# Optimization experiments

Measured on AMD Instinct MI355X. Metric: run time of the kernel, lower is better.

The kernel has to match this reference:

```python
import jax, jax.numpy as jnp
import numpy as np

K = 16  # kNN neighbors


def _knn(xb, k):
    # xb: [N, H] -> [N, k] nearest-neighbor indices (self excluded)
    sq = jnp.sum(xb * xb, axis=-1)
    d = sq[:, None] + sq[None, :] - 2.0 * (xb @ xb.T)  # squared distances [N, N]
    n = xb.shape[0]
    big = jnp.asarray(1e30, d.dtype)
    d = d + jnp.eye(n, dtype=d.dtype) * big  # mask self-loops
    _, idx = jax.lax.top_k(-d, k)
    return idx


def _edgeconv(h, W0, b0, W1, b1, k):
    # Dynamic kNN graph on current features + EdgeConv with 2-layer MLP, aggr='add'
    idx = jax.vmap(lambda xb: _knn(xb, k))(h)                 # [B, N, k]
    xj = jax.vmap(lambda xb, ib: xb[ib])(h, idx)              # [B, N, k, H] gather neighbors
    xi = jnp.broadcast_to(h[:, :, None, :], xj.shape)         # [B, N, k, H]
    m = jnp.concatenate([xi, xj - xi], axis=-1)               # [B, N, k, 2H]
    e = jax.nn.elu(m @ W0 + b0)
    e = jax.nn.elu(e @ W1 + b1)
    return jnp.sum(e, axis=2)                                 # 'add' aggregation over neighbors


def _forward(x, W_in0, b_in0, W_in1, b_in1, W_in2, b_in2,
             W_e0, b_e0, W_e1, b_e1,
             W_o0, b_o0, W_o1, b_o1, W_o2, b_o2):
    # input network (in_layers=3)
    h = jax.nn.elu(x @ W_in0 + b_in0)
    h = jax.nn.elu(h @ W_in1 + b_in1)
    h = jax.nn.elu(h @ W_in2 + b_in2)
    # agg_layers=2 blocks of dynamic-kNN EdgeConv
    for l in range(W_e0.shape[0]):
        h = _edgeconv(h, W_e0[l], b_e0[l], W_e1[l], b_e1[l], K)
    # global max pool over nodes of each graph (pool='max')
    g = jnp.max(h, axis=1)                                    # [B, H]
    # output network (out_layers=3)
    g = jax.nn.elu(g @ W_o0 + b_o0)
    g = jax.nn.elu(g @ W_o1 + b_o1)
    logits = g @ W_o2 + b_o2
    return jax.nn.log_softmax(logits, axis=1)


def setup_inputs() -> dict:
    key = jax.random.key(0)
    ks = jax.random.split(key, 8)
    B, N, F, H, C, A = 128, 512, 5, 64, 10, 2
    s = jnp.float32(0.1)

    def w(k, shape):
        return jax.random.normal(k, shape, jnp.float32) * s

    return {
        'x': jax.random.normal(ks[0], (B, N, F), jnp.float32),
        'W_in0': w(ks[1], (F, H)), 'b_in0': jnp.zeros((H,), jnp.float32),
        'W_in1': w(ks[2], (H, H)), 'b_in1': jnp.zeros((H,), jnp.float32),
        'W_in2': w(ks[3], (H, H)), 'b_in2': jnp.zeros((H,), jnp.float32),
        'W_e0': w(ks[4], (A, 2 * H, H)), 'b_e0': jnp.zeros((A, H), jnp.float32),
        'W_e1': w(ks[5], (A, H, H)), 'b_e1': jnp.zeros((A, H), jnp.float32),
        'W_o0': w(ks[6], (H, H)), 'b_o0': jnp.zeros((H,), jnp.float32),
        'W_o1': w(ks[7], (H, H)), 'b_o1': jnp.zeros((H,), jnp.float32),
        'W_o2': w(jax.random.fold_in(key, 99), (H, C)), 'b_o2': jnp.zeros((C,), jnp.float32),
    }


def reference(x, W_in0, b_in0, W_in1, b_in1, W_in2, b_in2,
              W_e0, b_e0, W_e1, b_e1,
              W_o0, b_o0, W_o1, b_o1, W_o2, b_o2):
    return _forward(x, W_in0, b_in0, W_in1, b_in1, W_in2, b_in2,
                    W_e0, b_e0, W_e1, b_e1,
                    W_o0, b_o0, W_o1, b_o1, W_o2, b_o2)
```

## Files before the change

kernel.cpp:

```cpp
#include <hip/hip_runtime.h>
#include <hip/hip_fp16.h>
#include <cmath>

typedef _Float16 f16;
typedef _Float16 f16x8 __attribute__((ext_vector_type(8)));
typedef float f32x4 __attribute__((ext_vector_type(4)));

#define B_ 128
#define N_ 512
#define H_ 64
#define K_ 16

__device__ __forceinline__ float elu_(float x) { return x > 0.f ? x : (__expf(x) - 1.f); }
__device__ __forceinline__ unsigned umin_(unsigned a, unsigned b) { return a < b ? a : b; }
__device__ __forceinline__ unsigned umax_(unsigned a, unsigned b) { return a > b ? a : b; }
__device__ __forceinline__ f32x4 mfma16(f16x8 a, f16x8 b, f32x4 c) {
    return __builtin_amdgcn_mfma_f32_16x16x32_f16(a, b, c, 0, 0, 0);
}
__device__ __forceinline__ f32x4 splat4(float v) { f32x4 r; r[0]=v; r[1]=v; r[2]=v; r[3]=v; return r; }
__device__ __forceinline__ unsigned mbcnt_(unsigned long long mask) {
    return __builtin_amdgcn_mbcnt_hi((unsigned)(mask >> 32),
           __builtin_amdgcn_mbcnt_lo((unsigned)mask, 0u));
}
__device__ __forceinline__ f16 hexp_(f16 x) {
    __half h = *(__half*)&x; h = hexp(h); return *(f16*)&h;
}
__device__ __forceinline__ f16x8 elu8h_(f16x8 x) {
    f16x8 z; f16x8 one;
    #pragma unroll
    for (int i = 0; i < 8; ++i) { z[i] = (f16)0.f; one[i] = (f16)1.f; }
    f16x8 mx = __builtin_elementwise_max(x, z);
    f16x8 mn = __builtin_elementwise_min(x, z);
    f16x8 e;
    #pragma unroll
    for (int i = 0; i < 8; ++i) e[i] = hexp_(mn[i]);
    return mx + e - one;
}
__device__ __forceinline__ unsigned wmax64_(unsigned v) {
    v = umax_(v, (unsigned)__builtin_amdgcn_update_dpp(0, (int)v, 0x111, 0xf, 0xf, true));
    v = umax_(v, (unsigned)__builtin_amdgcn_update_dpp(0, (int)v, 0x112, 0xf, 0xf, true));
    v = umax_(v, (unsigned)__builtin_amdgcn_update_dpp(0, (int)v, 0x114, 0xf, 0xf, true));
    v = umax_(v, (unsigned)__builtin_amdgcn_update_dpp(0, (int)v, 0x118, 0xf, 0xf, true));
    v = umax_(v, (unsigned)__builtin_amdgcn_update_dpp(0, (int)v, 0x142, 0xa, 0xf, true));
    v = umax_(v, (unsigned)__builtin_amdgcn_update_dpp(0, (int)v, 0x143, 0xc, 0xf, true));
    return (unsigned)__builtin_amdgcn_readlane((int)v, 63);
}
__device__ __forceinline__ float rsum16lo_(float x) {
    x += __int_as_float(__builtin_amdgcn_update_dpp(0, __float_as_int(x), 0x101, 0xf, 0xf, true));
    x += __int_as_float(__builtin_amdgcn_update_dpp(0, __float_as_int(x), 0x102, 0xf, 0xf, true));
    x += __int_as_float(__builtin_amdgcn_update_dpp(0, __float_as_int(x), 0x104, 0xf, 0xf, true));
    x += __int_as_float(__builtin_amdgcn_update_dpp(0, __float_as_int(x), 0x108, 0xf, 0xf, true));
    return x;
}

__global__ __launch_bounds__(256) void mlp_kernel(const float* __restrict__ x,
        const float* __restrict__ W0, const float* __restrict__ b0,
        const float* __restrict__ W1, const float* __restrict__ b1,
        const float* __restrict__ W2, const float* __restrict__ b2,
        f16* __restrict__ hout, float* __restrict__ sqout)
{
    __shared__ f16 tile[4][16*72];
    const int lane = threadIdx.x & 63, wid = threadIdx.x >> 6;
    const int m = lane & 15, q = lane >> 4;
    const int rowbase = blockIdx.x*64 + wid*16;
    f16* tw = tile[wid];

    f16x8 af0, af1;
    {
        const float* xp = x + (size_t)(rowbase + m)*5;
        #pragma unroll
        for (int jj = 0; jj < 8; ++jj) { int k = q*8+jj; af0[jj] = (k < 5) ? (f16)xp[k] : (f16)0.f; }
    }
    f32x4 acc[4];
    #pragma unroll
    for (int t = 0; t < 4; ++t) {
        f16x8 bf;
        #pragma unroll
        for (int jj = 0; jj < 8; ++jj) { int k = q*8+jj; bf[jj] = (k < 5) ? (f16)W0[k*64 + t*16+m] : (f16)0.f; }
        acc[t] = splat4(b0[t*16+m]);
        acc[t] = mfma16(af0, bf, acc[t]);
    }
    #pragma unroll
    for (int t = 0; t < 4; ++t)
        #pragma unroll
        for (int r = 0; r < 4; ++r)
            tw[(q*4+r)*72 + t*16+m] = (f16)elu_(acc[t][r]);
    __syncthreads();
    af0 = *(const f16x8*)(tw + m*72 + q*8);
    af1 = *(const f16x8*)(tw + m*72 + q*8 + 32);
    __syncthreads();

    #pragma unroll
    for (int t = 0; t < 4; ++t) {
        f16x8 bfa, bfb;
        #pragma unroll
        for (int jj = 0; jj < 8; ++jj) {
            bfa[jj] = (f16)W1[(q*8+jj)*64 + t*16+m];
            bfb[jj] = (f16)W1[(q*8+jj+32)*64 + t*16+m];
        }
        acc[t] = splat4(b1[t*16+m]);
        acc[t] = mfma16(af0, bfa, acc[t]);
        acc[t] = mfma16(af1, bfb, acc[t]);
    }
    #pragma unroll
    for (int t = 0; t < 4; ++t)
        #pragma unroll
        for (int r = 0; r < 4; ++r)
            tw[(q*4+r)*72 + t*16+m] = (f16)elu_(acc[t][r]);
    __syncthreads();
    af0 = *(const f16x8*)(tw + m*72 + q*8);
    af1 = *(const f16x8*)(tw + m*72 + q*8 + 32);

    #pragma unroll
    for (int t = 0; t < 4; ++t) {
        f16x8 bfa, bfb;
        #pragma unroll
        for (int jj = 0; jj < 8; ++jj) {
            bfa[jj] = (f16)W2[(q*8+jj)*64 + t*16+m];
            bfb[jj] = (f16)W2[(q*8+jj+32)*64 + t*16+m];
        }
        acc[t] = splat4(b2[t*16+m]);
        acc[t] = mfma16(af0, bfa, acc[t]);
        acc[t] = mfma16(af1, bfb, acc[t]);
    }
    float s[4] = {0.f,0.f,0.f,0.f};
    #pragma unroll
    for (int t = 0; t < 4; ++t)
        #pragma unroll
        for (int r = 0; r < 4; ++r) {
            float v = elu_(acc[t][r]);
            hout[(size_t)(rowbase + q*4 + r)*64 + t*16 + m] = (f16)v;
            s[r] += v*v;
        }
    #pragma unroll
    for (int r = 0; r < 4; ++r) s[r] = rsum16lo_(s[r]);
    if (m == 0) {
        #pragma unroll
        for (int r = 0; r < 4; ++r) sqout[rowbase + q*4 + r] = s[r];
    }
}

__global__ __launch_bounds__(512, 8) void knn_kernel(const f16* __restrict__ hin,
        const float* __restrict__ sq, int* __restrict__ idxout,
        const float* __restrict__ We, const float* __restrict__ be,
        f16* __restrict__ Pout, f16* __restrict__ Qout)
{
    __shared__ unsigned keys[16*512];
    const int lane = threadIdx.x & 63;
    const int wid  = threadIdx.x >> 6;
    const int m = lane & 15, q = lane >> 4;
    const int b  = blockIdx.x >> 5;
    const int rt = blockIdx.x & 31;
    const int rowbase = rt*16;
    const f16* hb = hin + (size_t)b*N_*H_;
    const float* sqb = sq + b*N_;

    f16x8 af0, af1;
    {
        const f16* Ap = hb + (size_t)(rowbase + m)*64 + q*8;
        af0 = *(const f16x8*)Ap;
        af1 = *(const f16x8*)(Ap + 32);
    }
    const int colb0 = wid*16;
    f16x8 bf0[4], bf1[4];
    float sc[4];
    #pragma unroll
    for (int cti = 0; cti < 4; ++cti) {
        const f16* Bp = hb + (size_t)(colb0 + cti*128 + m)*64 + q*8;
        bf0[cti] = *(const f16x8*)Bp;
        bf1[cti] = *(const f16x8*)(Bp + 32);
        sc[cti] = sqb[colb0 + cti*128 + m];
    }
    int base_r[4];
    #pragma unroll
    for (int r = 0; r < 4; ++r) {
        const int row = q*4 + r;
        base_r[r] = row*512 + ((colb0 + m) ^ (row << 1));
    }
    #pragma unroll
    for (int cti = 0; cti < 4; ++cti) {
        f32x4 acc = splat4(0.f);
        acc = mfma16(af0, bf0[cti], acc);
        acc = mfma16(af1, bf1[cti], acc);
        #pragma unroll
        for (int r = 0; r < 4; ++r) {
            float d = fmaf(-2.f, acc[r], sc[cti]);
            unsigned u = __float_as_uint(d);
            u ^= (0x80000000u | (unsigned)((int)u >> 31));
            unsigned key = (u & 0xFFFFFE00u) | (unsigned)(colb0 + cti*128 + m);
            keys[base_r[r] + cti*128] = key;
        }
    }
    __syncthreads();

    unsigned kk[2][8];
    #pragma unroll
    for (int rr = 0; rr < 2; ++rr) {
        const int ri = wid*2 + rr;
        *(uint4*)&kk[rr][0] = *(const uint4*)(keys + ri*512 + lane*4);
        *(uint4*)&kk[rr][4] = *(const uint4*)(keys + ri*512 + 256 + lane*4);
    }
    unsigned* scr = keys + wid*2*512;

    unsigned v[2];
    #pragma unroll
    for (int rr = 0; rr < 2; ++rr) {
        unsigned mn = kk[rr][0];
        #pragma unroll
        for (int s2 = 1; s2 < 8; ++s2) mn = umin_(mn, kk[rr][s2]);
        v[rr] = mn;
    }
    unsigned T[2] = {0u,0u};
    #pragma unroll
    for (int bit = 31; bit >= 9; --bit) {
        #pragma unroll
        for (int rr = 0; rr < 2; ++rr) {
            unsigned cand = T[rr] | (1u << bit);
            int c = __popcll(__ballot(v[rr] < cand));
            T[rr] = (c < 17) ? cand : T[rr];
        }
    }
    T[0] |= 511u; T[1] |= 511u;

    unsigned cnt[2];
    #pragma unroll
    for (int rr = 0; rr < 2; ++rr) {
        unsigned long long bal[8];
        #pragma unroll
        for (int s2 = 0; s2 < 8; ++s2) bal[s2] = __ballot(kk[rr][s2] <= T[rr]);
        unsigned base = 0;
        #pragma unroll
        for (int s2 = 0; s2 < 8; ++s2) {
            if (kk[rr][s2] <= T[rr]) {
                unsigned pos = base + mbcnt_(bal[s2]);
                if (pos < 64u) scr[rr*64 + pos] = kk[rr][s2];
            }
            base += (unsigned)__popcll(bal[s2]);
        }
        cnt[rr] = base;
    }

    #pragma unroll
    for (int rr = 0; rr < 2; ++rr) {
        const unsigned cc_ = umin_(cnt[rr], 64u);
        const int ri = wid*2 + rr;
        const unsigned rowglob = (unsigned)(rowbase + ri);
        bool act = lane < (int)cc_;
        unsigned mv = act ? scr[rr*64 + lane] : 0u;
        if (act && (mv & 511u) == rowglob) { act = false; mv = 0u; }
        int e = __popcll(__ballot(act)) - 16;
        while (e > 0) {
            unsigned mx = wmax64_(mv);
            if (mv == mx) { act = false; mv = 0u; }
            --e;
        }
        int* outp = idxout + ((size_t)b*N_ + rowglob)*K_;
        unsigned long long bal = __ballot(act);
        unsigned rank = mbcnt_(bal);
        if (act) outp[rank] = (int)(mv & 511u);
    }

    {
        const int t = wid & 3;
        f32x4 acc = (wid < 4) ? splat4(be[t*16+m]) : splat4(0.f);
        #pragma unroll
        for (int cc = 0; cc < 2; ++cc) {
            const f16x8 afc = cc ? af1 : af0;
            f16x8 bb;
            if (wid < 4) {
                #pragma unroll
                for (int jj = 0; jj < 8; ++jj) {
                    float wa = We[(q*8+jj+32*cc)*64 + t*16+m];
                    float wb = We[(q*8+jj+32*cc+64)*64 + t*16+m];
                    bb[jj] = (f16)(wa - wb);
                }
            } else {
                #pragma unroll
                for (int jj = 0; jj < 8; ++jj)
                    bb[jj] = (f16)We[(q*8+jj+32*cc+64)*64 + t*16+m];
            }
            acc = mfma16(afc, bb, acc);
        }
        f16* outp = (wid < 4) ? Pout : Qout;
        #pragma unroll
        for (int r = 0; r < 4; ++r)
            outp[((size_t)b*N_ + rowbase + q*4 + r)*64 + t*16 + m] = (f16)acc[r];
    }
}

__device__ __forceinline__ void edge_node_(size_t r0, f16x8 pa, f16x8 pb,
        f16x8 qa, f16x8 qb, const f16x8 (&bf)[2][4], const float (&bcol)[4],
        f16* __restrict__ out, float* __restrict__ sqout, int lane)
{
    f16x8 af0 = elu8h_(pa + qa);
    f16x8 af1 = elu8h_(pb + qb);
    f32x4 acc[4];
    #pragma unroll
    for (int t = 0; t < 4; ++t) acc[t] = splat4(bcol[t]);
    #pragma unroll
    for (int t = 0; t < 4; ++t) acc[t] = mfma16(af0, bf[0][t], acc[t]);
    #pragma unroll
    for (int t = 0; t < 4; ++t) acc[t] = mfma16(af1, bf[1][t], acc[t]);
    float ssum = 0.f;
    #pragma unroll
    for (int t = 0; t < 4; ++t) {
        float s = elu_(acc[t][0]) + elu_(acc[t][1]) + elu_(acc[t][2]) + elu_(acc[t][3]);
        s += __shfl_xor(s, 16);
        s += __shfl_xor(s, 32);
        if (lane < 16) out[r0*64 + t*16 + lane] = (f16)s;
        ssum += s*s;
    }
    ssum = rsum16lo_(ssum);
    if (lane == 0) sqout[r0] = ssum;
}

__global__ __launch_bounds__(256, 5) void edge_kernel(const f16* __restrict__ P,
        const f16* __restrict__ Q, const int* __restrict__ idx,
        const float* __restrict__ W1, const float* __restrict__ b1,
        f16* __restrict__ out, float* __restrict__ sqout)
{
    const int lane = threadIdx.x & 63;
    const int wid  = threadIdx.x >> 6;
    const int m = lane & 15, q = lane >> 4;

    f16x8 bf[2][4];
    #pragma unroll
    for (int cc = 0; cc < 2; ++cc)
        #pragma unroll
        for (int t = 0; t < 4; ++t)
            #pragma unroll
            for (int jj = 0; jj < 8; ++jj)
                bf[cc][t][jj] = (f16)W1[(q*8 + jj + 32*cc)*64 + t*16 + m];
    float bcol[4];
    #pragma unroll
    for (int t = 0; t < 4; ++t) bcol[t] = b1[t*16 + m];

    const int node0 = blockIdx.x*32 + wid*8;
    const int gbase = node0 & ~(N_-1);
    const int c0a = q*8, c0b = q*8 + 32;
    int jv[8];
    #pragma unroll
    for (int i = 0; i < 8; ++i) jv[i] = idx[(size_t)(node0 + i)*K_ + m];

    #pragma unroll
    for (int ip = 0; ip < 4; ++ip) {
        const size_t r0 = (size_t)(node0 + 2*ip);
        const size_t r1 = r0 + 1;
        const size_t g0 = (size_t)(gbase + jv[2*ip]);
        const size_t g1 = (size_t)(gbase + jv[2*ip+1]);
        f16x8 p0a = *(const f16x8*)(P + r0*64 + c0a);
        f16x8 p0b = *(const f16x8*)(P + r0*64 + c0b);
        f16x8 q0a = *(const f16x8*)(Q + g0*64 + c0a);
        f16x8 q0b = *(const f16x8*)(Q + g0*64 + c0b);
        f16x8 p1a = *(const f16x8*)(P + r1*64 + c0a);
        f16x8 p1b = *(const f16x8*)(P + r1*64 + c0b);
        f16x8 q1a = *(const f16x8*)(Q + g1*64 + c0a);
        f16x8 q1b = *(const f16x8*)(Q + g1*64 + c0b);
        edge_node_(r0, p0a, p0b, q0a, q0b, bf, bcol, out, sqout, lane);
        edge_node_(r1, p1a, p1b, q1a, q1b, bf, bcol, out, sqout, lane);
    }
}

__global__ __launch_bounds__(256) void final_kernel(const f16* __restrict__ hin,
        const float* __restrict__ Wo0, const float* __restrict__ bo0,
        const float* __restrict__ Wo1, const float* __restrict__ bo1,
        const float* __restrict__ Wo2, const float* __restrict__ bo2,
        float* __restrict__ out)
{
    __shared__ float smax[32][64];
    __shared__ float g0[64], g1[64], g2[64], part[4][64], lg[10];
    const int t = threadIdx.x;
    const int b = blockIdx.x;
    const int cg = t & 7, rg = t >> 3;

    float mx[8];
    #pragma unroll
    for (int e = 0; e < 8; ++e) mx[e] = -3.0e38f;
    #pragma unroll
    for (int i = 0; i < 16; ++i) {
        const int row = rg + i*32;
        f16x8 vv = *(const f16x8*)(hin + ((size_t)b*N_ + row)*64 + cg*8);
        #pragma unroll
        for (int e = 0; e < 8; ++e) mx[e] = fmaxf(mx[e], (float)vv[e]);
    }
    #pragma unroll
    for (int e = 0; e < 8; ++e) smax[rg][cg*8 + e] = mx[e];
    __syncthreads();
    for (int s = 16; s >= 1; s >>= 1) {
        if (rg < s) {
            #pragma unroll
            for (int e = 0; e < 8; ++e)
                smax[rg][cg*8+e] = fmaxf(smax[rg][cg*8+e], smax[rg+s][cg*8+e]);
        }
        __syncthreads();
    }
    if (t < 64) g0[t] = smax[0][t];
    __syncthreads();

    const int j = t & 63, p = t >> 6;
    {
        float a = 0.f;
        #pragma unroll
        for (int c = 0; c < 16; ++c) a += g0[p*16 + c]*Wo0[(p*16 + c)*64 + j];
        part[p][j] = a;
    }
    __syncthreads();
    if (t < 64) g1[t] = elu_(part[0][t] + part[1][t] + part[2][t] + part[3][t] + bo0[t]);
    __syncthreads();
    {
        float a = 0.f;
        #pragma unroll
        for (int c = 0; c < 16; ++c) a += g1[p*16 + c]*Wo1[(p*16 + c)*64 + j];
        part[p][j] = a;
    }
    __syncthreads();
    if (t < 64) g2[t] = elu_(part[0][t] + part[1][t] + part[2][t] + part[3][t] + bo1[t]);
    __syncthreads();
    if (t < 10) { float a = bo2[t]; for (int c = 0; c < 64; ++c) a += g2[c]*Wo2[c*10 + t]; lg[t] = a; }
    __syncthreads();
    if (t == 0) {
        float mxl = lg[0];
        for (int i = 1; i < 10; ++i) mxl = fmaxf(mxl, lg[i]);
        float s = 0.f;
        for (int i = 0; i < 10; ++i) s += expf(lg[i] - mxl);
        const float lse = mxl + logf(s);
        for (int i = 0; i < 10; ++i) out[b*10 + i] = lg[i] - lse;
    }
}

extern "C" void kernel_launch(void* const* d_in, const int* in_sizes, int n_in,
                              void* d_out, int out_size, void* d_ws, size_t ws_size,
                              hipStream_t stream) {
    const float* x     = (const float*)d_in[0];
    const float* W_in0 = (const float*)d_in[1];
    const float* b_in0 = (const float*)d_in[2];
    const float* W_in1 = (const float*)d_in[3];
    const float* b_in1 = (const float*)d_in[4];
    const float* W_in2 = (const float*)d_in[5];
    const float* b_in2 = (const float*)d_in[6];
    const float* W_e0  = (const float*)d_in[7];
    const float* b_e0  = (const float*)d_in[8];
    const float* W_e1  = (const float*)d_in[9];
    const float* b_e1  = (const float*)d_in[10];
    const float* Wo0   = (const float*)d_in[11];
    const float* bo0   = (const float*)d_in[12];
    const float* Wo1   = (const float*)d_in[13];
    const float* bo1   = (const float*)d_in[14];
    const float* Wo2   = (const float*)d_in[15];
    const float* bo2   = (const float*)d_in[16];

    char* ws = (char*)d_ws;
    f16*   hA   = (f16*)(ws);
    f16*   hB   = (f16*)(ws + 8388608);
    f16*   Pb   = (f16*)(ws + 16777216);
    f16*   Qb   = (f16*)(ws + 25165824);
    int*   idxb = (int*)(ws + 33554432);
    float* sqb  = (float*)(ws + 37748736);

    mlp_kernel<<<1024, 256, 0, stream>>>(x, W_in0, b_in0, W_in1, b_in1, W_in2, b_in2,
                                         hA, sqb);
    knn_kernel<<<4096, 512, 0, stream>>>(hA, sqb, idxb, W_e0, b_e0, Pb, Qb);
    edge_kernel<<<2048, 256, 0, stream>>>(Pb, Qb, idxb, W_e1, b_e1, hB, sqb);
    knn_kernel<<<4096, 512, 0, stream>>>(hB, sqb, idxb, W_e0 + 8192, b_e0 + 64, Pb, Qb);
    edge_kernel<<<2048, 256, 0, stream>>>(Pb, Qb, idxb, W_e1 + 4096, b_e1 + 64, hA, sqb);

    final_kernel<<<128, 256, 0, stream>>>(hA, Wo0, bo0, Wo1, bo1, Wo2, bo2, (float*)d_out);
}
```

Measured before the change: 285.3 us.

## Stage per-graph Q table in swizzled LDS for edge kernel neighbor gathers

The edge kernel now runs one 512-thread block per quarter graph. Each block copies that graph's full 512x64 fp16 Q matrix into XOR-swizzled shared memory, so the kNN neighbor gathers read LDS instead of scattered global memory. Each wave handles 16 nodes in a rolled loop. The trade-off is 64KB of LDS per block, which limits occupancy, plus each graph's Q being loaded four times (once per quarter-block). The edge kernel is small next to the kNN kernels.

```diff
diff --git a/kernel.cpp b/kernel.cpp
--- a/kernel.cpp
+++ b/kernel.cpp
@@ -288,40 +288,27 @@
     }
 }
 
-__device__ __forceinline__ void edge_node_(size_t r0, f16x8 pa, f16x8 pb,
-        f16x8 qa, f16x8 qb, const f16x8 (&bf)[2][4], const float (&bcol)[4],
-        f16* __restrict__ out, float* __restrict__ sqout, int lane)
-{
-    f16x8 af0 = elu8h_(pa + qa);
-    f16x8 af1 = elu8h_(pb + qb);
-    f32x4 acc[4];
-    #pragma unroll
-    for (int t = 0; t < 4; ++t) acc[t] = splat4(bcol[t]);
-    #pragma unroll
-    for (int t = 0; t < 4; ++t) acc[t] = mfma16(af0, bf[0][t], acc[t]);
-    #pragma unroll
-    for (int t = 0; t < 4; ++t) acc[t] = mfma16(af1, bf[1][t], acc[t]);
-    float ssum = 0.f;
-    #pragma unroll
-    for (int t = 0; t < 4; ++t) {
-        float s = elu_(acc[t][0]) + elu_(acc[t][1]) + elu_(acc[t][2]) + elu_(acc[t][3]);
-        s += __shfl_xor(s, 16);
-        s += __shfl_xor(s, 32);
-        if (lane < 16) out[r0*64 + t*16 + lane] = (f16)s;
-        ssum += s*s;
-    }
-    ssum = rsum16lo_(ssum);
-    if (lane == 0) sqout[r0] = ssum;
-}
-
-__global__ __launch_bounds__(256, 5) void edge_kernel(const f16* __restrict__ P,
+__global__ __launch_bounds__(512, 4) void edge_kernel(const f16* __restrict__ P,
         const f16* __restrict__ Q, const int* __restrict__ idx,
         const float* __restrict__ W1, const float* __restrict__ b1,
         f16* __restrict__ out, float* __restrict__ sqout)
 {
+    __shared__ f16 qlds[N_*H_];
     const int lane = threadIdx.x & 63;
     const int wid  = threadIdx.x >> 6;
     const int m = lane & 15, q = lane >> 4;
+    const int tid  = threadIdx.x;
+    const int b    = blockIdx.x >> 2;
+    const int quad = blockIdx.x & 3;
+    const int gbase = b * N_;
+
+    #pragma unroll
+    for (int p = 0; p < 8; ++p) {
+        const int L = tid + p*512;
+        const int j = L >> 3, c = L & 7;
+        f16x8 vv = *(const f16x8*)(Q + ((size_t)gbase + j)*64 + c*8);
+        *(f16x8*)(qlds + j*64 + ((c ^ (j & 7))*8)) = vv;
+    }
 
     f16x8 bf[2][4];
     #pragma unroll
@@ -334,30 +321,40 @@
     float bcol[4];
     #pragma unroll
     for (int t = 0; t < 4; ++t) bcol[t] = b1[t*16 + m];
-
-    const int node0 = blockIdx.x*32 + wid*8;
-    const int gbase = node0 & ~(N_-1);
-    const int c0a = q*8, c0b = q*8 + 32;
-    int jv[8];
-    #pragma unroll
-    for (int i = 0; i < 8; ++i) jv[i] = idx[(size_t)(node0 + i)*K_ + m];
-
-    #pragma unroll
-    for (int ip = 0; ip < 4; ++ip) {
-        const size_t r0 = (size_t)(node0 + 2*ip);
-        const size_t r1 = r0 + 1;
-        const size_t g0 = (size_t)(gbase + jv[2*ip]);
-        const size_t g1 = (size_t)(gbase + jv[2*ip+1]);
-        f16x8 p0a = *(const f16x8*)(P + r0*64 + c0a);
-        f16x8 p0b = *(const f16x8*)(P + r0*64 + c0b);
-        f16x8 q0a = *(const f16x8*)(Q + g0*64 + c0a);
-        f16x8 q0b = *(const f16x8*)(Q + g0*64 + c0b);
-        f16x8 p1a = *(const f16x8*)(P + r1*64 + c0a);
-        f16x8 p1b = *(const f16x8*)(P + r1*64 + c0b);
-        f16x8 q1a = *(const f16x8*)(Q + g1*64 + c0a);
-        f16x8 q1b = *(const f16x8*)(Q + g1*64 + c0b);
-        edge_node_(r0, p0a, p0b, q0a, q0b, bf, bcol, out, sqout, lane);
-        edge_node_(r1, p1a, p1b, q1a, q1b, bf, bcol, out, sqout, lane);
+    __syncthreads();
+
+    const int node0 = gbase + quad*128 + wid*16;
+    int jv[16];
+    #pragma unroll
+    for (int i = 0; i < 16; ++i) jv[i] = idx[(size_t)(node0 + i)*K_ + m];
+
+    for (int i = 0; i < 16; ++i) {
+        const size_t r0 = (size_t)(node0 + i);
+        const int j = jv[i];
+        f16x8 pa = *(const f16x8*)(P + r0*64 + q*8);
+        f16x8 pb = *(const f16x8*)(P + r0*64 + q*8 + 32);
+        f16x8 qa = *(const f16x8*)(qlds + j*64 + ((q       ^ (j & 7))*8));
+        f16x8 qb = *(const f16x8*)(qlds + j*64 + (((q + 4) ^ (j & 7))*8));
+        f16x8 af0 = elu8h_(pa + qa);
+        f16x8 af1 = elu8h_(pb + qb);
+        f32x4 acc[4];
+        #pragma unroll
+        for (int t = 0; t < 4; ++t) acc[t] = splat4(bcol[t]);
+        #pragma unroll
+        for (int t = 0; t < 4; ++t) acc[t] = mfma16(af0, bf[0][t], acc[t]);
+        #pragma unroll
+        for (int t = 0; t < 4; ++t) acc[t] = mfma16(af1, bf[1][t], acc[t]);
+        float ssum = 0.f;
+        #pragma unroll
+        for (int t = 0; t < 4; ++t) {
+            float s = elu_(acc[t][0]) + elu_(acc[t][1]) + elu_(acc[t][2]) + elu_(acc[t][3]);
+            s += __shfl_xor(s, 16);
+            s += __shfl_xor(s, 32);
+            if (lane < 16) out[r0*64 + t*16 + lane] = (f16)s;
+            ssum += s*s;
+        }
+        ssum = rsum16lo_(ssum);
+        if (lane == 0) sqout[r0] = ssum;
     }
 }
 
@@ -460,9 +457,9 @@
     mlp_kernel<<<1024, 256, 0, stream>>>(x, W_in0, b_in0, W_in1, b_in1, W_in2, b_in2,
                                          hA, sqb);
     knn_kernel<<<4096, 512, 0, stream>>>(hA, sqb, idxb, W_e0, b_e0, Pb, Qb);
-    edge_kernel<<<2048, 256, 0, stream>>>(Pb, Qb, idxb, W_e1, b_e1, hB, sqb);
+    edge_kernel<<<512, 512, 0, stream>>>(Pb, Qb, idxb, W_e1, b_e1, hB, sqb);
     knn_kernel<<<4096, 512, 0, stream>>>(hB, sqb, idxb, W_e0 + 8192, b_e0 + 64, Pb, Qb);
-    edge_kernel<<<2048, 256, 0, stream>>>(Pb, Qb, idxb, W_e1 + 4096, b_e1 + 64, hA, sqb);
+    edge_kernel<<<512, 512, 0, stream>>>(Pb, Qb, idxb, W_e1 + 4096, b_e1 + 64, hA, sqb);
 
     final_kernel<<<128, 256, 0, stream>>>(hA, Wo0, bo0, Wo1, bo1, Wo2, bo2, (float*)d_out);
 }
```

New measurement: 295.4 us. +3.5%, slower.

## Fuse global max-pool into last edge kernel via atomicMax on order-preserving keys

Applied to the files above, without the earlier changes.

The final EdgeConv layer no longer writes per-node features and squared norms. Each wave keeps a running per-channel max, encoded as an order-preserving unsigned key, and commits it with atomicMax into a small per-graph pool buffer. The second knn kernel zeroes that buffer before use. The final kernel now only decodes the pooled vector and runs the small output MLP with 64 threads, which removes a full read of the node features. In exchange it adds global atomics (8 waves per graph channel slot per block) and relies on the pool zeroing in the knn kernel finishing before the edge kernel runs.

```diff
diff --git a/kernel.cpp b/kernel.cpp
--- a/kernel.cpp
+++ b/kernel.cpp
@@ -51,6 +51,13 @@
     x += __int_as_float(__builtin_amdgcn_update_dpp(0, __float_as_int(x), 0x104, 0xf, 0xf, true));
     x += __int_as_float(__builtin_amdgcn_update_dpp(0, __float_as_int(x), 0x108, 0xf, 0xf, true));
     return x;
+}
+__device__ __forceinline__ unsigned fmap_(float x) {
+    unsigned u = __float_as_uint(x);
+    return ((int)u >= 0) ? (u | 0x80000000u) : ~u;
+}
+__device__ __forceinline__ float funmap_(unsigned m) {
+    return (m & 0x80000000u) ? __uint_as_float(m ^ 0x80000000u) : __uint_as_float(~m);
 }
 
 __global__ __launch_bounds__(256) void mlp_kernel(const float* __restrict__ x,
@@ -143,7 +150,8 @@
 __global__ __launch_bounds__(512, 8) void knn_kernel(const f16* __restrict__ hin,
         const float* __restrict__ sq, int* __restrict__ idxout,
         const float* __restrict__ We, const float* __restrict__ be,
-        f16* __restrict__ Pout, f16* __restrict__ Qout)
+        f16* __restrict__ Pout, f16* __restrict__ Qout,
+        unsigned* __restrict__ pool)
 {
     __shared__ unsigned keys[16*512];
     const int lane = threadIdx.x & 63;
@@ -154,6 +162,9 @@
     const int rowbase = rt*16;
     const f16* hb = hin + (size_t)b*N_*H_;
     const float* sqb = sq + b*N_;
+
+    if (pool != nullptr && blockIdx.x < 16)
+        pool[blockIdx.x*512 + threadIdx.x] = 0u;
 
     f16x8 af0, af1;
     {
@@ -288,9 +299,11 @@
     }
 }
 
+template<bool DOPOOL>
 __device__ __forceinline__ void edge_node_(size_t r0, f16x8 pa, f16x8 pb,
         f16x8 qa, f16x8 qb, const f16x8 (&bf)[2][4], const float (&bcol)[4],
-        f16* __restrict__ out, float* __restrict__ sqout, int lane)
+        f16* __restrict__ out, float* __restrict__ sqout, int lane,
+        unsigned (&pmax)[4])
 {
     f16x8 af0 = elu8h_(pa + qa);
     f16x8 af1 = elu8h_(pb + qb);
@@ -307,17 +320,25 @@
         float s = elu_(acc[t][0]) + elu_(acc[t][1]) + elu_(acc[t][2]) + elu_(acc[t][3]);
         s += __shfl_xor(s, 16);
         s += __shfl_xor(s, 32);
-        if (lane < 16) out[r0*64 + t*16 + lane] = (f16)s;
-        ssum += s*s;
-    }
-    ssum = rsum16lo_(ssum);
-    if (lane == 0) sqout[r0] = ssum;
-}
-
+        if (DOPOOL) {
+            pmax[t] = umax_(pmax[t], fmap_(s));
+        } else {
+            if (lane < 16) out[r0*64 + t*16 + lane] = (f16)s;
+            ssum += s*s;
+        }
+    }
+    if (!DOPOOL) {
+        ssum = rsum16lo_(ssum);
+        if (lane == 0) sqout[r0] = ssum;
+    }
+}
+
+template<bool DOPOOL>
 __global__ __launch_bounds__(256, 5) void edge_kernel(const f16* __restrict__ P,
         const f16* __restrict__ Q, const int* __restrict__ idx,
         const float* __restrict__ W1, const float* __restrict__ b1,
-        f16* __restrict__ out, float* __restrict__ sqout)
+        f16* __restrict__ out, float* __restrict__ sqout,
+        unsigned* __restrict__ pool)
 {
     const int lane = threadIdx.x & 63;
     const int wid  = threadIdx.x >> 6;
@@ -342,6 +363,7 @@
     #pragma unroll
     for (int i = 0; i < 8; ++i) jv[i] = idx[(size_t)(node0 + i)*K_ + m];
 
+    unsigned pmax[4] = {0u,0u,0u,0u};
     #pragma unroll
     for (int ip = 0; ip < 4; ++ip) {
         const size_t r0 = (size_t)(node0 + 2*ip);
@@ -356,65 +378,41 @@
         f16x8 p1b = *(const f16x8*)(P + r1*64 + c0b);
         f16x8 q1a = *(const f16x8*)(Q + g1*64 + c0a);
         f16x8 q1b = *(const f16x8*)(Q + g1*64 + c0b);
-        edge_node_(r0, p0a, p0b, q0a, q0b, bf, bcol, out, sqout, lane);
-        edge_node_(r1, p1a, p1b, q1a, q1b, bf, bcol, out, sqout, lane);
-    }
-}
-
-__global__ __launch_bounds__(256) void final_kernel(const f16* __restrict__ hin,
+        edge_node_<DOPOOL>(r0, p0a, p0b, q0a, q0b, bf, bcol, out, sqout, lane, pmax);
+        edge_node_<DOPOOL>(r1, p1a, p1b, q1a, q1b, bf, bcol, out, sqout, lane, pmax);
+    }
+    if (DOPOOL) {
+        const int bg = gbase >> 9;
+        if (lane < 16) {
+            #pragma unroll
+            for (int t = 0; t < 4; ++t)
+                atomicMax(pool + bg*64 + t*16 + lane, pmax[t]);
+        }
+    }
+}
+
+__global__ __launch_bounds__(64) void final_kernel(const unsigned* __restrict__ pool,
         const float* __restrict__ Wo0, const float* __restrict__ bo0,
         const float* __restrict__ Wo1, const float* __restrict__ bo1,
         const float* __restrict__ Wo2, const float* __restrict__ bo2,
         float* __restrict__ out)
 {
-    __shared__ float smax[32][64];
-    __shared__ float g0[64], g1[64], g2[64], part[4][64], lg[10];
+    __shared__ float g0[64], g1[64], g2[64], lg[10];
     const int t = threadIdx.x;
     const int b = blockIdx.x;
-    const int cg = t & 7, rg = t >> 3;
-
-    float mx[8];
-    #pragma unroll
-    for (int e = 0; e < 8; ++e) mx[e] = -3.0e38f;
-    #pragma unroll
-    for (int i = 0; i < 16; ++i) {
-        const int row = rg + i*32;
-        f16x8 vv = *(const f16x8*)(hin + ((size_t)b*N_ + row)*64 + cg*8);
-        #pragma unroll
-        for (int e = 0; e < 8; ++e) mx[e] = fmaxf(mx[e], (float)vv[e]);
-    }
-    #pragma unroll
-    for (int e = 0; e < 8; ++e) smax[rg][cg*8 + e] = mx[e];
-    __syncthreads();
-    for (int s = 16; s >= 1; s >>= 1) {
-        if (rg < s) {
-            #pragma unroll
-            for (int e = 0; e < 8; ++e)
-                smax[rg][cg*8+e] = fmaxf(smax[rg][cg*8+e], smax[rg+s][cg*8+e]);
-        }
-        __syncthreads();
-    }
-    if (t < 64) g0[t] = smax[0][t];
-    __syncthreads();
-
-    const int j = t & 63, p = t >> 6;
+    g0[t] = funmap_(pool[b*64 + t]);
+    __syncthreads();
     {
-        float a = 0.f;
-        #pragma unroll
-        for (int c = 0; c < 16; ++c) a += g0[p*16 + c]*Wo0[(p*16 + c)*64 + j];
-        part[p][j] = a;
-    }
-    __syncthreads();
-    if (t < 64) g1[t] = elu_(part[0][t] + part[1][t] + part[2][t] + part[3][t] + bo0[t]);
+        float a = bo0[t];
+        for (int c = 0; c < 64; ++c) a += g0[c]*Wo0[c*64 + t];
+        g1[t] = elu_(a);
+    }
     __syncthreads();
     {
-        float a = 0.f;
-        #pragma unroll
-        for (int c = 0; c < 16; ++c) a += g1[p*16 + c]*Wo1[(p*16 + c)*64 + j];
-        part[p][j] = a;
-    }
-    __syncthreads();
-    if (t < 64) g2[t] = elu_(part[0][t] + part[1][t] + part[2][t] + part[3][t] + bo1[t]);
+        float a = bo1[t];
+        for (int c = 0; c < 64; ++c) a += g1[c]*Wo1[c*64 + t];
+        g2[t] = elu_(a);
+    }
     __syncthreads();
     if (t < 10) { float a = bo2[t]; for (int c = 0; c < 64; ++c) a += g2[c]*Wo2[c*10 + t]; lg[t] = a; }
     __syncthreads();
@@ -450,19 +448,20 @@
     const float* bo2   = (const float*)d_in[16];
 
     char* ws = (char*)d_ws;
-    f16*   hA   = (f16*)(ws);
-    f16*   hB   = (f16*)(ws + 8388608);
-    f16*   Pb   = (f16*)(ws + 16777216);
-    f16*   Qb   = (f16*)(ws + 25165824);
-    int*   idxb = (int*)(ws + 33554432);
-    float* sqb  = (float*)(ws + 37748736);
+    f16*      hA   = (f16*)(ws);
+    f16*      hB   = (f16*)(ws + 8388608);
+    f16*      Pb   = (f16*)(ws + 16777216);
+    f16*      Qb   = (f16*)(ws + 25165824);
+    int*      idxb = (int*)(ws + 33554432);
+    float*    sqb  = (float*)(ws + 37748736);
+    unsigned* pool = (unsigned*)(ws + 38010880);
 
     mlp_kernel<<<1024, 256, 0, stream>>>(x, W_in0, b_in0, W_in1, b_in1, W_in2, b_in2,
                                          hA, sqb);
-    knn_kernel<<<4096, 512, 0, stream>>>(hA, sqb, idxb, W_e0, b_e0, Pb, Qb);
-    edge_kernel<<<2048, 256, 0, stream>>>(Pb, Qb, idxb, W_e1, b_e1, hB, sqb);
-    knn_kernel<<<4096, 512, 0, stream>>>(hB, sqb, idxb, W_e0 + 8192, b_e0 + 64, Pb, Qb);
-    edge_kernel<<<2048, 256, 0, stream>>>(Pb, Qb, idxb, W_e1 + 4096, b_e1 + 64, hA, sqb);
-
-    final_kernel<<<128, 256, 0, stream>>>(hA, Wo0, bo0, Wo1, bo1, Wo2, bo2, (float*)d_out);
-}
+    knn_kernel<<<4096, 512, 0, stream>>>(hA, sqb, idxb, W_e0, b_e0, Pb, Qb, nullptr);
+    edge_kernel<false><<<2048, 256, 0, stream>>>(Pb, Qb, idxb, W_e1, b_e1, hB, sqb, nullptr);
+    knn_kernel<<<4096, 512, 0, stream>>>(hB, sqb, idxb, W_e0 + 8192, b_e0 + 64, Pb, Qb, pool);
+    edge_kernel<true><<<2048, 256, 0, stream>>>(Pb, Qb, idxb, W_e1 + 4096, b_e1 + 64,
+                                                nullptr, nullptr, pool);
+    final_kernel<<<128, 64, 0, stream>>>(pool, Wo0, bo0, Wo1, bo1, Wo2, bo2, (float*)d_out);
+}
```

Result: slower. 398.2 us (+39.5%).
